# Performance work log

Measured on AMD Instinct MI355X. Metric: run time of the kernel, lower is better.

## Reference

```python
import jax, jax.numpy as jnp
import numpy as np

N_NODES = 50000
N_EDGES = 600000
IN_DIM = 128
HID = 128
OUT_DIM = 40
NUM_REL = 3
LN_EPS = 1e-5


def layer_norm(x, g, b):
    mu = jnp.mean(x, axis=-1, keepdims=True)
    var = jnp.var(x, axis=-1, keepdims=True)
    return (x - mu) * jax.lax.rsqrt(var + LN_EPS) * g + b


def rgcn_conv(x, edge_index, edge_type, w_rel, w_root, bias, aggr):
    """PyG-style RGCNConv: out = x @ W_root + bias + sum_r aggr_r(x_src @ W_r)."""
    src, dst = edge_index[0], edge_index[1]
    out = x @ w_root + bias                      # [N, F_out]
    for r in range(NUM_REL):                     # small fixed relation loop
        h = x @ w_rel[r]                         # transform-then-gather: [N, F_out]
        msg = h[src]                             # [E, F_out]
        mask = (edge_type == r)[:, None]
        if aggr == 'add':
            msg = jnp.where(mask, msg, 0.0)
            agg = jax.ops.segment_sum(msg, dst, num_segments=N_NODES)
        else:  # 'max'; empty segments -> 0 (matches PyG scatter_reduce include_self=False over zeros)
            msg = jnp.where(mask, msg, -jnp.inf)
            agg = jax.ops.segment_max(msg, dst, num_segments=N_NODES)
            agg = jnp.where(jnp.isfinite(agg), agg, 0.0)
        out = out + agg
    return out


def setup_inputs() -> dict:
    key = jax.random.key(0)
    ks = jax.random.split(key, 16)
    f32 = jnp.float32
    def lin(k, fan_in, shape):
        return jax.random.normal(k, shape, dtype=f32) / np.sqrt(fan_in)
    inp = {
        'x': jax.random.normal(ks[0], (N_NODES, IN_DIM), dtype=f32),
        'edge_index': jax.random.randint(ks[1], (2, N_EDGES), 0, N_NODES),
        'edge_type': jax.random.randint(ks[2], (N_EDGES,), 0, NUM_REL),
        # conv1
        'w1_rel': lin(ks[3], IN_DIM, (NUM_REL, IN_DIM, HID)),
        'w1_root': lin(ks[4], IN_DIM, (IN_DIM, HID)),
        'b1': jnp.zeros((HID,), f32),
        'ln1_g': jnp.ones((HID,), f32), 'ln1_b': jnp.zeros((HID,), f32),
        # conv2
        'w2_rel': lin(ks[5], HID, (NUM_REL, HID, HID)),
        'w2_root': lin(ks[6], HID, (HID, HID)),
        'b2': jnp.zeros((HID,), f32),
        'ln2_g': jnp.ones((HID,), f32), 'ln2_b': jnp.zeros((HID,), f32),
        # classifier
        'cw1': lin(ks[7], HID, (HID, HID)), 'cb1': jnp.zeros((HID,), f32),
        'cln1_g': jnp.ones((HID,), f32), 'cln1_b': jnp.zeros((HID,), f32),
        'cw2': lin(ks[8], HID, (HID, HID // 2)), 'cb2': jnp.zeros((HID // 2,), f32),
        'cln2_g': jnp.ones((HID // 2,), f32), 'cln2_b': jnp.zeros((HID // 2,), f32),
        'cw3': lin(ks[9], HID // 2, (HID // 2, OUT_DIM)), 'cb3': jnp.zeros((OUT_DIM,), f32),
    }
    return inp


def reference(x, edge_index, edge_type,
              w1_rel, w1_root, b1, ln1_g, ln1_b,
              w2_rel, w2_root, b2, ln2_g, ln2_b,
              cw1, cb1, cln1_g, cln1_b,
              cw2, cb2, cln2_g, cln2_b,
              cw3, cb3):
    # eval mode: edge dropout and feature dropout are identity
    h = rgcn_conv(x, edge_index, edge_type, w1_rel, w1_root, b1, 'add')
    h = jax.nn.relu(layer_norm(h, ln1_g, ln1_b))
    x1 = h
    h = rgcn_conv(x1, edge_index, edge_type, w2_rel, w2_root, b2, 'max')
    h = jax.nn.relu(layer_norm(h, ln2_g, ln2_b))
    h = h + x1 * 0.2
    # classifier MLP
    h = jax.nn.gelu(layer_norm(h @ cw1 + cb1, cln1_g, cln1_b), approximate=False)
    h = jax.nn.gelu(layer_norm(h @ cw2 + cb2, cln2_g, cln2_b), approximate=False)
    h = h @ cw3 + cb3
    return jax.nn.log_softmax(h, axis=1)
```

## Files before the change

kernel.cpp:

```cpp
#include <hip/hip_runtime.h>
#include <hip/hip_bf16.h>
#include <math.h>


typedef __attribute__((ext_vector_type(8))) short bf16x8;
typedef __attribute__((ext_vector_type(4))) float f32x4;
typedef unsigned short ushort_t;

__device__ __forceinline__ ushort_t bf16rne(float v) {
    unsigned u = __float_as_uint(v);
    return (ushort_t)((u + 0x7FFFu + ((u >> 16) & 1u)) >> 16);
}

__device__ __forceinline__ void split_bf16(float v, ushort_t& h, ushort_t& l) {
    ushort_t hu = bf16rne(v);
    float hf = __uint_as_float((unsigned)hu << 16);
    h = hu;
    l = bf16rne(v - hf);
}

__device__ __forceinline__ float bf2f(unsigned u16) {
    return __uint_as_float(u16 << 16);
}

__device__ __forceinline__ float4 unpack_bf4(uint2 u) {
    return make_float4(bf2f(u.x & 0xFFFFu), bf2f(u.x >> 16),
                       bf2f(u.y & 0xFFFFu), bf2f(u.y >> 16));
}

__device__ __forceinline__ uint2 pack_bf4(float4 v) {
    uint2 o;
    o.x = (unsigned)bf16rne(v.x) | ((unsigned)bf16rne(v.y) << 16);
    o.y = (unsigned)bf16rne(v.z) | ((unsigned)bf16rne(v.w) << 16);
    return o;
}

__device__ __forceinline__ void conv_body128(const float* __restrict__ W,
                                             ushort_t* __restrict__ out,
                                             int idx) {
    constexpr int NCF = 8;
    constexpr size_t PST = (size_t)4 * NCF * 512;
    int l = idx & 63;
    int cf = (idx >> 6) & 7;
    int ks = idx >> 9;
    int col = cf * 16 + (l & 15);
    int k0 = ks * 32 + (l >> 4) * 8;
    size_t base = (((size_t)ks * NCF + cf) * 64 + l) * 8;
#pragma unroll
    for (int j = 0; j < 8; ++j) {
        ushort_t h, lo_;
        split_bf16(W[(size_t)(k0 + j) * 128 + col], h, lo_);
        out[base + j] = h;
        out[PST + base + j] = lo_;
    }
}

__global__ __launch_bounds__(256) void convert_all(
    const float* __restrict__ w1_root, const float* __restrict__ w1_rel,
    const float* __restrict__ w2_root, const float* __restrict__ w2_rel,
    const float* __restrict__ cw1, const float* __restrict__ cw2,
    ushort_t* __restrict__ wfb) {
    int b = blockIdx.x;
    if (b < 72) {
        const float* src;
        int slot;
        if (b < 8)       { slot = 0;              src = w1_root; }
        else if (b < 32) { int r = (b - 8) >> 3;  slot = 1 + r; src = w1_rel + (size_t)r * 16384; }
        else if (b < 40) { slot = 4;              src = w2_root; }
        else if (b < 64) { int r = (b - 40) >> 3; slot = 5 + r; src = w2_rel + (size_t)r * 16384; }
        else             { slot = 8;              src = cw1; }
        int lb = (b < 8) ? b : (b < 32) ? ((b - 8) & 7) : (b < 40) ? (b - 32)
               : (b < 64) ? ((b - 40) & 7) : (b - 64);
        conv_body128(src, wfb + (size_t)slot * 32768, lb * 256 + threadIdx.x);
    } else {
        constexpr int NCF = 4;
        constexpr size_t PST = (size_t)4 * NCF * 512;
        int idx = (b - 72) * 256 + threadIdx.x;
        ushort_t* out = wfb + (size_t)9 * 32768;
        int l = idx & 63;
        int cf = (idx >> 6) & 3;
        int ks = idx >> 8;
        int col = cf * 16 + (l & 15);
        int k0 = ks * 32 + (l >> 4) * 8;
        size_t base = (((size_t)ks * NCF + cf) * 64 + l) * 8;
#pragma unroll
        for (int j = 0; j < 8; ++j) {
            ushort_t h, lo_;
            split_bf16(cw2[(size_t)(k0 + j) * 64 + col], h, lo_);
            out[base + j] = h;
            out[PST + base + j] = lo_;
        }
    }
}

__global__ __launch_bounds__(256) void x2bf(const float* __restrict__ x,
                                            ushort_t* __restrict__ xh, int n4) {
    int g = blockIdx.x * 256 + threadIdx.x;
    if (g >= n4) return;
    float4 v = ((const float4*)x)[g];
    ((uint2*)xh)[g] = pack_bf4(v);
}

template <int NCOL, int NSEG, int FUSE>
__global__ __launch_bounds__(256, 3) void gemm_bf(
    const ushort_t* __restrict__ A0, const ushort_t* __restrict__ A1,
    const ushort_t* __restrict__ A2, const ushort_t* __restrict__ A3,
    const ushort_t* __restrict__ wfrag, const float* __restrict__ bias,
    const float* __restrict__ lng, const float* __restrict__ lnb,
    void* __restrict__ Yv, int M) {
    constexpr int NCF = NCOL / 16;
    constexpr int WF = NCOL / 32;
    constexpr int PST = 4 * NCF * 512;
    constexpr int WSEG = 2 * PST;
    constexpr int RS = NCOL * 4 + 16;
    constexpr int EPB = 64 * RS;
    constexpr int SMEM_BYTES = (EPB > 16384) ? EPB : 16384;
    __shared__ __align__(16) char smem[SMEM_BYTES];
    char (*lds)[8192] = (char(*)[8192])smem;

    const int tid = threadIdx.x;
    const int wv = tid >> 6, lane = tid & 63, l15 = lane & 15, lg = lane >> 4;
    const int rowgrp = wv >> 1, colgrp = wv & 1;
    const int row0 = blockIdx.x * 64;
    const ushort_t* As[4] = {A0, A1, A2, A3};

    f32x4 acc[2][WF];
#pragma unroll
    for (int xf = 0; xf < 2; ++xf)
#pragma unroll
        for (int wf = 0; wf < WF; ++wf) acc[xf][wf] = (f32x4){0.f, 0.f, 0.f, 0.f};

    uint4 regs[2];

    auto LOADSTAGE = [&](int ch) {
        const ushort_t* __restrict__ A = As[ch >> 1];
        int kcb = (ch & 1) * 128;
#pragma unroll
        for (int i = 0; i < 2; ++i) {
            int s = tid + i * 256;
            int r = s >> 3, c16 = s & 7;
            int gr = row0 + r;
            uint4 v = make_uint4(0u, 0u, 0u, 0u);
            if (gr < M)
                v = *(const uint4*)((const char*)A + (size_t)gr * 256 + kcb + c16 * 16);
            regs[i] = v;
        }
    };

    auto WRITESTAGE = [&](int buf) {
        char* L = lds[buf];
#pragma unroll
        for (int i = 0; i < 2; ++i) {
            int s = tid + i * 256;
            int r = s >> 3, c16 = s & 7;
            int byte = (r * 128 + c16 * 16) ^ ((r & 7) << 4);
            *(uint4*)(L + byte) = regs[i];
        }
    };

    auto COMPUTE = [&](int ch, int buf) {
        int seg = ch >> 1, half = ch & 1;
        const ushort_t* __restrict__ ws = wfrag + (size_t)seg * WSEG;
        const char* L = lds[buf];
#pragma unroll
        for (int kk = 0; kk < 2; ++kk) {
            int ks = half * 2 + kk;
            bf16x8 xh[2];
#pragma unroll
            for (int xf = 0; xf < 2; ++xf) {
                int r = rowgrp * 32 + xf * 16 + l15;
                int byte = (r * 128 + kk * 64 + lg * 16) ^ ((r & 7) << 4);
                xh[xf] = *(const bf16x8*)(L + byte);
            }
            bf16x8 wh[WF], wl[WF];
#pragma unroll
            for (int wf = 0; wf < WF; ++wf) {
                size_t off = (((size_t)ks * NCF + colgrp * WF + wf) * 64 + lane) * 8;
                wh[wf] = *(const bf16x8*)(ws + off);
                wl[wf] = *(const bf16x8*)(ws + PST + off);
            }
#pragma unroll
            for (int xf = 0; xf < 2; ++xf)
#pragma unroll
                for (int wf = 0; wf < WF; ++wf) {
                    acc[xf][wf] = __builtin_amdgcn_mfma_f32_16x16x32_bf16(
                        wh[wf], xh[xf], acc[xf][wf], 0, 0, 0);
                    acc[xf][wf] = __builtin_amdgcn_mfma_f32_16x16x32_bf16(
                        wl[wf], xh[xf], acc[xf][wf], 0, 0, 0);
                }
        }
    };

    constexpr int CH = 2 * NSEG;
    LOADSTAGE(0);
    WRITESTAGE(0);
    __syncthreads();
    for (int ch = 0; ch < CH; ++ch) {
        if (ch + 1 < CH) LOADSTAGE(ch + 1);
        COMPUTE(ch, ch & 1);
        __syncthreads();
        if (ch + 1 < CH) WRITESTAGE((ch + 1) & 1);
        __syncthreads();
    }

    {
        float4 bv[WF];
#pragma unroll
        for (int wf = 0; wf < WF; ++wf) {
            int col = colgrp * (NCOL / 2) + wf * 16 + lg * 4;
            bv[wf] = bias ? *(const float4*)(bias + col)
                          : make_float4(0.f, 0.f, 0.f, 0.f);
        }
#pragma unroll
        for (int xf = 0; xf < 2; ++xf) {
            int r = rowgrp * 32 + xf * 16 + l15;
#pragma unroll
            for (int wf = 0; wf < WF; ++wf) {
                int col = colgrp * (NCOL / 2) + wf * 16 + lg * 4;
                float4 o;
                o.x = acc[xf][wf][0] + bv[wf].x;
                o.y = acc[xf][wf][1] + bv[wf].y;
                o.z = acc[xf][wf][2] + bv[wf].z;
                o.w = acc[xf][wf][3] + bv[wf].w;
                *(float4*)(smem + r * RS + col * 4) = o;
            }
        }
    }
    __syncthreads();

    if (FUSE >= 1 && FUSE <= 3) {
        constexpr int CPT = NCOL / 4;
        int r = tid >> 2, seg = tid & 3;
        char* rp = smem + r * RS + seg * CPT * 4;
        float s = 0.f, sq = 0.f;
        float4 vv[CPT / 4];
#pragma unroll
        for (int j = 0; j < CPT / 4; ++j) {
            float4 v = *(const float4*)(rp + j * 16);
            vv[j] = v;
            s += (v.x + v.y) + (v.z + v.w);
            sq += (v.x * v.x + v.y * v.y) + (v.z * v.z + v.w * v.w);
        }
        s += __shfl_xor(s, 1, 64); sq += __shfl_xor(sq, 1, 64);
        s += __shfl_xor(s, 2, 64); sq += __shfl_xor(sq, 2, 64);
        float mu = s * (1.f / NCOL);
        float var = sq * (1.f / NCOL) - mu * mu;
        float rstd = rsqrtf(var + 1e-5f);
#pragma unroll
        for (int j = 0; j < CPT / 4; ++j) {
            int c0 = seg * CPT + j * 4;
            float4 v = vv[j];
            float4 gg = *(const float4*)(lng + c0);
            float4 bb = *(const float4*)(lnb + c0);
            float y0 = (v.x - mu) * rstd * gg.x + bb.x;
            float y1 = (v.y - mu) * rstd * gg.y + bb.y;
            float y2 = (v.z - mu) * rstd * gg.z + bb.z;
            float y3 = (v.w - mu) * rstd * gg.w + bb.w;
            if (FUSE == 1) {
                y0 = fmaxf(y0, 0.f); y1 = fmaxf(y1, 0.f);
                y2 = fmaxf(y2, 0.f); y3 = fmaxf(y3, 0.f);
            } else {
                y0 = 0.5f * y0 * (1.f + erff(y0 * 0.70710678118654752f));
                y1 = 0.5f * y1 * (1.f + erff(y1 * 0.70710678118654752f));
                y2 = 0.5f * y2 * (1.f + erff(y2 * 0.70710678118654752f));
                y3 = 0.5f * y3 * (1.f + erff(y3 * 0.70710678118654752f));
            }
            vv[j] = make_float4(y0, y1, y2, y3);
        }
        __syncthreads();
        if (FUSE == 3) {
#pragma unroll
            for (int j = 0; j < CPT / 4; ++j) *(float4*)(rp + j * 16) = vv[j];
        } else {
#pragma unroll
            for (int j = 0; j < CPT / 4; ++j) {
                int c0 = seg * CPT + j * 4;
                *(uint2*)(smem + r * RS + 2 * c0) = pack_bf4(vv[j]);
            }
        }
        __syncthreads();
    }

    if (FUSE == 4) {
        constexpr int SL = 64 * (NCOL / 8);
#pragma unroll
        for (int i = 0; i < SL / 256; ++i) {
            int slot = tid + i * 256;
            int rr = slot / (NCOL / 8), c16 = slot % (NCOL / 8);
            int gr = row0 + rr;
            if (gr < M) {
                float4 a = *(const float4*)(smem + rr * RS + c16 * 32);
                float4 b = *(const float4*)(smem + rr * RS + c16 * 32 + 16);
                uint4 o;
                uint2 pa = pack_bf4(a), pb = pack_bf4(b);
                o.x = pa.x; o.y = pa.y; o.z = pb.x; o.w = pb.y;
                *(uint4*)((char*)Yv + (size_t)gr * (NCOL * 2) + c16 * 16) = o;
            }
        }
    } else {
        constexpr int OUTB = (FUSE == 0 || FUSE == 3) ? NCOL * 4 : NCOL * 2;
        constexpr int RP = OUTB / 16;
        constexpr int SL = 64 * RP;
#pragma unroll
        for (int i = 0; i < SL / 256; ++i) {
            int slot = tid + i * 256;
            int rr = slot / RP, c16 = slot % RP;
            int gr = row0 + rr;
            if (gr < M)
                *(uint4*)((char*)Yv + (size_t)gr * OUTB + c16 * 16) =
                    *(const uint4*)(smem + rr * RS + c16 * 16);
        }
    }
}

__global__ __launch_bounds__(256, 3) void gemm_conv2(
    const ushort_t* __restrict__ X, const ushort_t* __restrict__ wfb,
    const float* __restrict__ b2, float* __restrict__ accOut,
    ushort_t* __restrict__ H0, ushort_t* __restrict__ H1,
    ushort_t* __restrict__ H2, int M) {
    constexpr int NCF = 8, WF = 4;
    constexpr int PST = 4 * NCF * 512;
    constexpr int RS = 128 * 4 + 16;
    __shared__ __align__(16) char smem[16384 + 64 * RS];
    char* Xs = smem;
    char* ep = smem + 16384;

    const int tid = threadIdx.x;
    const int wv = tid >> 6, lane = tid & 63, l15 = lane & 15, lg = lane >> 4;
    const int rowgrp = wv >> 1, colgrp = wv & 1;
    const int row0 = blockIdx.x * 64;

#pragma unroll
    for (int i = 0; i < 4; ++i) {
        int s = tid + i * 256;
        int r = s >> 4, c16 = s & 15;
        int gr = row0 + r;
        uint4 v = make_uint4(0u, 0u, 0u, 0u);
        if (gr < M) v = *(const uint4*)((const char*)X + (size_t)gr * 256 + c16 * 16);
        int byte = (r * 256 + c16 * 16) ^ ((r & 7) << 4);
        *(uint4*)(Xs + byte) = v;
    }
    __syncthreads();

    ushort_t* Hs[3] = {H0, H1, H2};
    for (int set = 0; set < 4; ++set) {
        const ushort_t* __restrict__ ws = wfb + (size_t)(4 + set) * 32768;
        f32x4 acc[2][WF];
#pragma unroll
        for (int xf = 0; xf < 2; ++xf)
#pragma unroll
            for (int wf = 0; wf < WF; ++wf) acc[xf][wf] = (f32x4){0.f, 0.f, 0.f, 0.f};
#pragma unroll
        for (int ks = 0; ks < 4; ++ks) {
            bf16x8 xh[2];
#pragma unroll
            for (int xf = 0; xf < 2; ++xf) {
                int r = rowgrp * 32 + xf * 16 + l15;
                int byte = (r * 256 + ks * 64 + lg * 16) ^ ((r & 7) << 4);
                xh[xf] = *(const bf16x8*)(Xs + byte);
            }
            bf16x8 wh[WF], wl[WF];
#pragma unroll
            for (int wf = 0; wf < WF; ++wf) {
                size_t off = (((size_t)ks * NCF + colgrp * WF + wf) * 64 + lane) * 8;
                wh[wf] = *(const bf16x8*)(ws + off);
                wl[wf] = *(const bf16x8*)(ws + PST + off);
            }
#pragma unroll
            for (int xf = 0; xf < 2; ++xf)
#pragma unroll
                for (int wf = 0; wf < WF; ++wf) {
                    acc[xf][wf] = __builtin_amdgcn_mfma_f32_16x16x32_bf16(
                        wh[wf], xh[xf], acc[xf][wf], 0, 0, 0);
                    acc[xf][wf] = __builtin_amdgcn_mfma_f32_16x16x32_bf16(
                        wl[wf], xh[xf], acc[xf][wf], 0, 0, 0);
                }
        }
        __syncthreads();
        {
            float4 bv[WF];
#pragma unroll
            for (int wf = 0; wf < WF; ++wf) {
                int col = colgrp * 64 + wf * 16 + lg * 4;
                bv[wf] = (set == 0) ? *(const float4*)(b2 + col)
                                    : make_float4(0.f, 0.f, 0.f, 0.f);
            }
#pragma unroll
            for (int xf = 0; xf < 2; ++xf) {
                int r = rowgrp * 32 + xf * 16 + l15;
#pragma unroll
                for (int wf = 0; wf < WF; ++wf) {
                    int col = colgrp * 64 + wf * 16 + lg * 4;
                    float4 o;
                    o.x = acc[xf][wf][0] + bv[wf].x;
                    o.y = acc[xf][wf][1] + bv[wf].y;
                    o.z = acc[xf][wf][2] + bv[wf].z;
                    o.w = acc[xf][wf][3] + bv[wf].w;
                    *(float4*)(ep + r * RS + col * 4) = o;
                }
            }
        }
        __syncthreads();
        if (set == 0) {
#pragma unroll
            for (int i = 0; i < 8; ++i) {
                int slot = tid + i * 256;
                int rr = slot >> 5, c16 = slot & 31;
                int gr = row0 + rr;
                if (gr < M)
                    *(uint4*)((char*)accOut + (size_t)gr * 512 + c16 * 16) =
                        *(const uint4*)(ep + rr * RS + c16 * 16);
            }
        } else {
            ushort_t* H = Hs[set - 1];
#pragma unroll
            for (int i = 0; i < 4; ++i) {
                int slot = tid + i * 256;
                int rr = slot >> 4, c16 = slot & 15;
                int gr = row0 + rr;
                if (gr < M) {
                    float4 a = *(const float4*)(ep + rr * RS + c16 * 32);
                    float4 b = *(const float4*)(ep + rr * RS + c16 * 32 + 16);
                    uint2 pa = pack_bf4(a), pb = pack_bf4(b);
                    uint4 o; o.x = pa.x; o.y = pa.y; o.z = pb.x; o.w = pb.y;
                    *(uint4*)((char*)H + (size_t)gr * 256 + c16 * 16) = o;
                }
            }
        }
    }
}

__global__ __launch_bounds__(256) void hist3_kernel(const int* __restrict__ edst,
                                                    const int* __restrict__ etype,
                                                    int* __restrict__ deg3, int E) {
    int e = blockIdx.x * 256 + threadIdx.x;
    if (e < E) atomicAdd(&deg3[edst[e] * 3 + etype[e]], 1);
}

__global__ __launch_bounds__(256) void degtot_kernel(const int* __restrict__ deg3,
                                                     int* __restrict__ degtot, int N) {
    int n = blockIdx.x * 256 + threadIdx.x;
    if (n < N) degtot[n] = deg3[n * 3] + deg3[n * 3 + 1] + deg3[n * 3 + 2];
}

__global__ __launch_bounds__(256) void scan_block(const int* __restrict__ in,
                                                  int* __restrict__ out,
                                                  int* __restrict__ sums, int n) {
    __shared__ int s[256];
    int g = blockIdx.x * 256 + threadIdx.x;
    int v = (g < n) ? in[g] : 0;
    s[threadIdx.x] = v;
    __syncthreads();
    int acc = v;
    for (int off = 1; off < 256; off <<= 1) {
        int t = (threadIdx.x >= off) ? s[threadIdx.x - off] : 0;
        __syncthreads();
        acc += t;
        s[threadIdx.x] = acc;
        __syncthreads();
    }
    if (g < n) out[g] = acc - v;
    if (threadIdx.x == 255 && sums) sums[blockIdx.x] = acc;
}

__global__ __launch_bounds__(256) void scan_add(int* __restrict__ out,
                                                const int* __restrict__ topex,
                                                int n, int total) {
    int g = blockIdx.x * 256 + threadIdx.x;
    if (g < n) out[g] += topex[blockIdx.x];
    if (g == 0) out[n] = total;
}

__global__ __launch_bounds__(256) void ranges_kernel(
    const int* __restrict__ rowptr, const int* __restrict__ deg3,
    int4* __restrict__ ranges, int* __restrict__ cursor3, int N) {
    int n = blockIdx.x * 256 + threadIdx.x;
    if (n >= N) return;
    int b = rowptr[n];
    int d0 = deg3[n * 3], d1 = deg3[n * 3 + 1];
    int4 r;
    r.x = b; r.y = b + d0; r.z = b + d0 + d1; r.w = rowptr[n + 1];
    ranges[n] = r;
    cursor3[n * 3] = r.x; cursor3[n * 3 + 1] = r.y; cursor3[n * 3 + 2] = r.z;
}

__global__ __launch_bounds__(256) void fill3_kernel(
    const int* __restrict__ esrc, const int* __restrict__ edst,
    const int* __restrict__ etype, int* __restrict__ cursor3,
    int* __restrict__ colidx, int E) {
    int e = blockIdx.x * 256 + threadIdx.x;
    if (e >= E) return;
    int pos = atomicAdd(&cursor3[edst[e] * 3 + etype[e]], 1);
    colidx[pos] = esrc[e];
}

__device__ __forceinline__ float4 gather_sum_bf(const ushort_t* __restrict__ XH,
                                                const int* __restrict__ colidx,
                                                int beg, int end, int l) {
    float4 a = make_float4(0.f, 0.f, 0.f, 0.f);
    int e = beg;
    for (; e + 4 <= end; e += 4) {
        int s0 = colidx[e], s1 = colidx[e + 1];
        int s2 = colidx[e + 2], s3 = colidx[e + 3];
        float4 v0 = unpack_bf4(*(const uint2*)(XH + (size_t)s0 * 128 + l * 4));
        float4 v1 = unpack_bf4(*(const uint2*)(XH + (size_t)s1 * 128 + l * 4));
        float4 v2 = unpack_bf4(*(const uint2*)(XH + (size_t)s2 * 128 + l * 4));
        float4 v3 = unpack_bf4(*(const uint2*)(XH + (size_t)s3 * 128 + l * 4));
        a.x += (v0.x + v1.x) + (v2.x + v3.x);
        a.y += (v0.y + v1.y) + (v2.y + v3.y);
        a.z += (v0.z + v1.z) + (v2.z + v3.z);
        a.w += (v0.w + v1.w) + (v2.w + v3.w);
    }
    for (; e < end; ++e) {
        float4 v = unpack_bf4(*(const uint2*)(XH + (size_t)colidx[e] * 128 + l * 4));
        a.x += v.x; a.y += v.y; a.z += v.z; a.w += v.w;
    }
    return a;
}

__global__ __launch_bounds__(256) void agg3_add(
    const ushort_t* __restrict__ xh, const int4* __restrict__ ranges,
    const int* __restrict__ colidx, ushort_t* __restrict__ S0,
    ushort_t* __restrict__ S1, ushort_t* __restrict__ S2, int N) {
    int node = blockIdx.x * 8 + (threadIdx.x >> 5);
    int l = threadIdx.x & 31;
    if (node >= N) return;
    int4 rg = ranges[node];
    float4 a0 = gather_sum_bf(xh, colidx, rg.x, rg.y, l);
    float4 a1 = gather_sum_bf(xh, colidx, rg.y, rg.z, l);
    float4 a2 = gather_sum_bf(xh, colidx, rg.z, rg.w, l);
    *(uint2*)(S0 + (size_t)node * 128 + l * 4) = pack_bf4(a0);
    *(uint2*)(S1 + (size_t)node * 128 + l * 4) = pack_bf4(a1);
    *(uint2*)(S2 + (size_t)node * 128 + l * 4) = pack_bf4(a2);
}

__device__ __forceinline__ float4 gather_max_bf(const ushort_t* __restrict__ H,
                                                const int* __restrict__ colidx,
                                                int beg, int end, int l) {
    float4 m = make_float4(-INFINITY, -INFINITY, -INFINITY, -INFINITY);
    int e = beg;
    for (; e + 4 <= end; e += 4) {
        int s0 = colidx[e], s1 = colidx[e + 1];
        int s2 = colidx[e + 2], s3 = colidx[e + 3];
        float4 v0 = unpack_bf4(*(const uint2*)(H + (size_t)s0 * 128 + l * 4));
        float4 v1 = unpack_bf4(*(const uint2*)(H + (size_t)s1 * 128 + l * 4));
        float4 v2 = unpack_bf4(*(const uint2*)(H + (size_t)s2 * 128 + l * 4));
        float4 v3 = unpack_bf4(*(const uint2*)(H + (size_t)s3 * 128 + l * 4));
        m.x = fmaxf(m.x, fmaxf(fmaxf(v0.x, v1.x), fmaxf(v2.x, v3.x)));
        m.y = fmaxf(m.y, fmaxf(fmaxf(v0.y, v1.y), fmaxf(v2.y, v3.y)));
        m.z = fmaxf(m.z, fmaxf(fmaxf(v0.z, v1.z), fmaxf(v2.z, v3.z)));
        m.w = fmaxf(m.w, fmaxf(fmaxf(v0.w, v1.w), fmaxf(v2.w, v3.w)));
    }
    for (; e < end; ++e) {
        float4 v = unpack_bf4(*(const uint2*)(H + (size_t)colidx[e] * 128 + l * 4));
        m.x = fmaxf(m.x, v.x); m.y = fmaxf(m.y, v.y);
        m.z = fmaxf(m.z, v.z); m.w = fmaxf(m.w, v.w);
    }
    m.x = (m.x > -3e38f) ? m.x : 0.f;
    m.y = (m.y > -3e38f) ? m.y : 0.f;
    m.z = (m.z > -3e38f) ? m.z : 0.f;
    m.w = (m.w > -3e38f) ? m.w : 0.f;
    return m;
}

__global__ __launch_bounds__(256) void maxagg_ln(
    const ushort_t* __restrict__ H0, const ushort_t* __restrict__ H1,
    const ushort_t* __restrict__ H2, const int4* __restrict__ ranges,
    const int* __restrict__ colidx, const float* __restrict__ acc,
    const ushort_t* __restrict__ resid, const float* __restrict__ g,
    const float* __restrict__ b, ushort_t* __restrict__ outH, int N) {
    int node = blockIdx.x * 8 + (threadIdx.x >> 5);
    int l = threadIdx.x & 31;
    if (node >= N) return;
    int4 rg = ranges[node];
    float4 m0 = gather_max_bf(H0, colidx, rg.x, rg.y, l);
    float4 m1 = gather_max_bf(H1, colidx, rg.y, rg.z, l);
    float4 m2 = gather_max_bf(H2, colidx, rg.z, rg.w, l);
    float4 a = *(const float4*)(acc + (size_t)node * 128 + l * 4);
    a.x += m0.x + m1.x + m2.x;
    a.y += m0.y + m1.y + m2.y;
    a.z += m0.z + m1.z + m2.z;
    a.w += m0.w + m1.w + m2.w;
    float s = (a.x + a.y) + (a.z + a.w);
    float sq = (a.x * a.x + a.y * a.y) + (a.z * a.z + a.w * a.w);
#pragma unroll
    for (int off = 16; off; off >>= 1) {
        s += __shfl_xor(s, off, 64);
        sq += __shfl_xor(sq, off, 64);
    }
    float mu = s * (1.f / 128.f);
    float var = sq * (1.f / 128.f) - mu * mu;
    float rstd = rsqrtf(var + 1e-5f);
    float4 gg = *(const float4*)(g + l * 4);
    float4 bb = *(const float4*)(b + l * 4);
    float4 rv = unpack_bf4(*(const uint2*)(resid + (size_t)node * 128 + l * 4));
    float4 y;
    y.x = fmaxf((a.x - mu) * rstd * gg.x + bb.x, 0.f) + 0.2f * rv.x;
    y.y = fmaxf((a.y - mu) * rstd * gg.y + bb.y, 0.f) + 0.2f * rv.y;
    y.z = fmaxf((a.z - mu) * rstd * gg.z + bb.z, 0.f) + 0.2f * rv.z;
    y.w = fmaxf((a.w - mu) * rstd * gg.w + bb.w, 0.f) + 0.2f * rv.w;
    *(uint2*)(outH + (size_t)node * 128 + l * 4) = pack_bf4(y);
}

__global__ __launch_bounds__(256) void gemm40_lsm(const float* __restrict__ X,
                                                  const float* __restrict__ W,
                                                  const float* __restrict__ bias,
                                                  float* __restrict__ Y, int M) {
    __shared__ float Xs[64][65];
    __shared__ float Ws[64 * 40];
    __shared__ float Ys[64][41];
    __shared__ float mx_[64], ls_[64];
    const int tid = threadIdx.x;
    const int row0 = blockIdx.x * 64;
    for (int i = tid; i < 64 * 40; i += 256) Ws[i] = W[i];
#pragma unroll
    for (int i = 0; i < 4; ++i) {
        int slot = tid + i * 256;
        int r = slot >> 4, c4 = slot & 15;
        float4 v = make_float4(0.f, 0.f, 0.f, 0.f);
        if (row0 + r < M) v = *(const float4*)(X + (size_t)(row0 + r) * 64 + c4 * 4);
        Xs[r][c4 * 4 + 0] = v.x; Xs[r][c4 * 4 + 1] = v.y;
        Xs[r][c4 * 4 + 2] = v.z; Xs[r][c4 * 4 + 3] = v.w;
    }
    __syncthreads();
    const int row = tid >> 2, cg = (tid & 3) * 10;
    float acc[10];
#pragma unroll
    for (int j = 0; j < 10; ++j) acc[j] = 0.f;
#pragma unroll 8
    for (int k = 0; k < 64; ++k) {
        float xv = Xs[row][k];
#pragma unroll
        for (int j = 0; j < 10; ++j) acc[j] = fmaf(xv, Ws[k * 40 + cg + j], acc[j]);
    }
#pragma unroll
    for (int j = 0; j < 10; ++j) Ys[row][cg + j] = acc[j] + bias[cg + j];
    __syncthreads();
    if (tid < 64) {
        float mx = -INFINITY;
#pragma unroll 8
        for (int c = 0; c < 40; ++c) mx = fmaxf(mx, Ys[tid][c]);
        float sum = 0.f;
#pragma unroll 8
        for (int c = 0; c < 40; ++c) sum += __expf(Ys[tid][c] - mx);
        mx_[tid] = mx;
        ls_[tid] = logf(sum);
    }
    __syncthreads();
#pragma unroll
    for (int i = 0; i < 10; ++i) {
        int slot = tid + i * 256;
        int r = slot / 40, c = slot % 40;
        int gr = row0 + r;
        if (gr < M) Y[(size_t)gr * 40 + c] = Ys[r][c] - mx_[r] - ls_[r];
    }
}

extern "C" void kernel_launch(void* const* d_in, const int* in_sizes, int n_in,
                              void* d_out, int out_size, void* d_ws, size_t ws_size,
                              hipStream_t stream) {
    const float* x       = (const float*)d_in[0];
    const int*   eidx    = (const int*)d_in[1];
    const int*   etype   = (const int*)d_in[2];
    const float* w1_rel  = (const float*)d_in[3];
    const float* w1_root = (const float*)d_in[4];
    const float* b1      = (const float*)d_in[5];
    const float* ln1_g   = (const float*)d_in[6];
    const float* ln1_b   = (const float*)d_in[7];
    const float* w2_rel  = (const float*)d_in[8];
    const float* w2_root = (const float*)d_in[9];
    const float* b2      = (const float*)d_in[10];
    const float* ln2_g   = (const float*)d_in[11];
    const float* ln2_b   = (const float*)d_in[12];
    const float* cw1     = (const float*)d_in[13];
    const float* cb1     = (const float*)d_in[14];
    const float* cln1_g  = (const float*)d_in[15];
    const float* cln1_b  = (const float*)d_in[16];
    const float* cw2     = (const float*)d_in[17];
    const float* cb2     = (const float*)d_in[18];
    const float* cln2_g  = (const float*)d_in[19];
    const float* cln2_b  = (const float*)d_in[20];
    const float* cw3     = (const float*)d_in[21];
    const float* cb3     = (const float*)d_in[22];

    const int N = in_sizes[0] / 128;
    const int E = in_sizes[1] / 2;
    const int* esrc = eidx;
    const int* edst = eidx + E;

    const size_t HB = (size_t)N * 256;
    char* base = (char*)d_ws;
    ushort_t* S0 = (ushort_t*)(base + 0 * HB);
    ushort_t* S1 = (ushort_t*)(base + 1 * HB);
    ushort_t* S2 = (ushort_t*)(base + 2 * HB);
    ushort_t* X1 = (ushort_t*)(base + 3 * HB);
    float*    AC = (float*)   (base + 4 * HB);
    char*     B3 = base + 6 * HB;

    int* rowptr  = (int*)B3;
    int* degtot  = rowptr + (N + 1);
    int* deg3    = degtot + N;
    int* cursor3 = deg3 + 3 * N;
    int* bsums   = cursor3 + 3 * N;
    int* btop    = bsums + 256;
    int4* ranges = (int4*)(((uintptr_t)(btop + 256) + 15) & ~(uintptr_t)15);
    int* colidx  = (int*)(ranges + N);
    ushort_t* wfb = (ushort_t*)(((uintptr_t)(colidx + E) + 255) & ~(uintptr_t)255);
    auto WSLOT = [&](int i) { return wfb + (size_t)i * 32768; };
    ushort_t* xh = (ushort_t*)(((uintptr_t)(wfb + 10 * 32768) + 255) & ~(uintptr_t)255);
    ushort_t* h2 = xh;
    ushort_t* C1 = S0;
    float*    C2 = (float*)S1;

    const dim3 blk(256);
    const int gGemm = (N + 63) / 64;
    const int gAgg  = (N + 7) / 8;
    const int gEdge = (E + 255) / 256;
    const int gNode = (N + 255) / 256;
    const int nScanB = (N + 255) / 256;
    const int gX2  = (N * 32 + 255) / 256;

    hipMemsetAsync(deg3, 0, (size_t)3 * N * sizeof(int), stream);
    hist3_kernel<<<gEdge, blk, 0, stream>>>(edst, etype, deg3, E);
    degtot_kernel<<<gNode, blk, 0, stream>>>(deg3, degtot, N);
    scan_block<<<nScanB, blk, 0, stream>>>(degtot, rowptr, bsums, N);
    scan_block<<<1, blk, 0, stream>>>(bsums, btop, nullptr, nScanB);
    scan_add<<<nScanB, blk, 0, stream>>>(rowptr, btop, N, E);
    ranges_kernel<<<gNode, blk, 0, stream>>>(rowptr, deg3, ranges, cursor3, N);
    fill3_kernel<<<gEdge, blk, 0, stream>>>(esrc, edst, etype, cursor3, colidx, E);

    convert_all<<<76, blk, 0, stream>>>(w1_root, w1_rel, w2_root, w2_rel,
                                        cw1, cw2, wfb);
    x2bf<<<gX2, blk, 0, stream>>>(x, xh, N * 32);

    agg3_add<<<gAgg, blk, 0, stream>>>(xh, ranges, colidx, S0, S1, S2, N);
    gemm_bf<128, 4, 1><<<gGemm, blk, 0, stream>>>(
        xh, S0, S1, S2, WSLOT(0), b1, ln1_g, ln1_b, X1, N);

    gemm_conv2<<<gGemm, blk, 0, stream>>>(X1, wfb, b2, AC, S0, S1, S2, N);
    maxagg_ln<<<gAgg, blk, 0, stream>>>(S0, S1, S2, ranges, colidx, AC,
                                        X1, ln2_g, ln2_b, h2, N);

    gemm_bf<128, 1, 2><<<gGemm, blk, 0, stream>>>(
        h2, h2, h2, h2, WSLOT(8), cb1, cln1_g, cln1_b, C1, N);
    gemm_bf<64, 1, 3><<<gGemm, blk, 0, stream>>>(
        C1, C1, C1, C1, WSLOT(9), cb2, cln2_g, cln2_b, C2, N);
    gemm40_lsm<<<gGemm, blk, 0, stream>>>(C2, cw3, cb3, (float*)d_out, N);
}
```

Before: 274.5 us.

## Store conv2 root accumulator as bf16 and batch all four weight sets per k-step

```diff
diff --git a/kernel.cpp b/kernel.cpp
--- a/kernel.cpp
+++ b/kernel.cpp
@@ -313,17 +313,16 @@
     }
 }
 
-__global__ __launch_bounds__(256, 3) void gemm_conv2(
+__global__ __launch_bounds__(256, 2) void gemm_conv2(
     const ushort_t* __restrict__ X, const ushort_t* __restrict__ wfb,
-    const float* __restrict__ b2, float* __restrict__ accOut,
+    const float* __restrict__ b2, ushort_t* __restrict__ ACbf,
     ushort_t* __restrict__ H0, ushort_t* __restrict__ H1,
     ushort_t* __restrict__ H2, int M) {
     constexpr int NCF = 8, WF = 4;
     constexpr int PST = 4 * NCF * 512;
-    constexpr int RS = 128 * 4 + 16;
-    __shared__ __align__(16) char smem[16384 + 64 * RS];
+    constexpr int RS2 = 256 + 16;
+    __shared__ __align__(16) char smem[2 * 64 * RS2];
     char* Xs = smem;
-    char* ep = smem + 16384;
 
     const int tid = threadIdx.x;
     const int wv = tid >> 6, lane = tid & 63, l15 = lane & 15, lg = lane >> 4;
@@ -342,23 +341,27 @@
     }
     __syncthreads();
 
-    ushort_t* Hs[3] = {H0, H1, H2};
-    for (int set = 0; set < 4; ++set) {
-        const ushort_t* __restrict__ ws = wfb + (size_t)(4 + set) * 32768;
-        f32x4 acc[2][WF];
+    f32x4 acc[4][2][WF];
+#pragma unroll
+    for (int set = 0; set < 4; ++set)
 #pragma unroll
         for (int xf = 0; xf < 2; ++xf)
 #pragma unroll
-            for (int wf = 0; wf < WF; ++wf) acc[xf][wf] = (f32x4){0.f, 0.f, 0.f, 0.f};
-#pragma unroll
-        for (int ks = 0; ks < 4; ++ks) {
-            bf16x8 xh[2];
-#pragma unroll
-            for (int xf = 0; xf < 2; ++xf) {
-                int r = rowgrp * 32 + xf * 16 + l15;
-                int byte = (r * 256 + ks * 64 + lg * 16) ^ ((r & 7) << 4);
-                xh[xf] = *(const bf16x8*)(Xs + byte);
-            }
+            for (int wf = 0; wf < WF; ++wf)
+                acc[set][xf][wf] = (f32x4){0.f, 0.f, 0.f, 0.f};
+
+#pragma unroll
+    for (int ks = 0; ks < 4; ++ks) {
+        bf16x8 xh[2];
+#pragma unroll
+        for (int xf = 0; xf < 2; ++xf) {
+            int r = rowgrp * 32 + xf * 16 + l15;
+            int byte = (r * 256 + ks * 64 + lg * 16) ^ ((r & 7) << 4);
+            xh[xf] = *(const bf16x8*)(Xs + byte);
+        }
+#pragma unroll
+        for (int set = 0; set < 4; ++set) {
+            const ushort_t* __restrict__ ws = wfb + (size_t)(4 + set) * 32768;
             bf16x8 wh[WF], wl[WF];
 #pragma unroll
             for (int wf = 0; wf < WF; ++wf) {
@@ -370,21 +373,22 @@
             for (int xf = 0; xf < 2; ++xf)
 #pragma unroll
                 for (int wf = 0; wf < WF; ++wf) {
-                    acc[xf][wf] = __builtin_amdgcn_mfma_f32_16x16x32_bf16(
-                        wh[wf], xh[xf], acc[xf][wf], 0, 0, 0);
-                    acc[xf][wf] = __builtin_amdgcn_mfma_f32_16x16x32_bf16(
-                        wl[wf], xh[xf], acc[xf][wf], 0, 0, 0);
+                    acc[set][xf][wf] = __builtin_amdgcn_mfma_f32_16x16x32_bf16(
+                        wh[wf], xh[xf], acc[set][xf][wf], 0, 0, 0);
+                    acc[set][xf][wf] = __builtin_amdgcn_mfma_f32_16x16x32_bf16(
+                        wl[wf], xh[xf], acc[set][xf][wf], 0, 0, 0);
                 }
         }
-        __syncthreads();
-        {
-            float4 bv[WF];
-#pragma unroll
-            for (int wf = 0; wf < WF; ++wf) {
-                int col = colgrp * 64 + wf * 16 + lg * 4;
-                bv[wf] = (set == 0) ? *(const float4*)(b2 + col)
-                                    : make_float4(0.f, 0.f, 0.f, 0.f);
-            }
+    }
+    __syncthreads();
+
+    ushort_t* outs[4] = {ACbf, H0, H1, H2};
+#pragma unroll
+    for (int round = 0; round < 2; ++round) {
+#pragma unroll
+        for (int s2 = 0; s2 < 2; ++s2) {
+            int set = round * 2 + s2;
+            char* tile = smem + s2 * (64 * RS2);
 #pragma unroll
             for (int xf = 0; xf < 2; ++xf) {
                 int r = rowgrp * 32 + xf * 16 + l15;
@@ -392,41 +396,35 @@
                 for (int wf = 0; wf < WF; ++wf) {
                     int col = colgrp * 64 + wf * 16 + lg * 4;
                     float4 o;
-                    o.x = acc[xf][wf][0] + bv[wf].x;
-                    o.y = acc[xf][wf][1] + bv[wf].y;
-                    o.z = acc[xf][wf][2] + bv[wf].z;
-                    o.w = acc[xf][wf][3] + bv[wf].w;
-                    *(float4*)(ep + r * RS + col * 4) = o;
+                    o.x = acc[set][xf][wf][0];
+                    o.y = acc[set][xf][wf][1];
+                    o.z = acc[set][xf][wf][2];
+                    o.w = acc[set][xf][wf][3];
+                    if (set == 0) {
+                        float4 bv = *(const float4*)(b2 + col);
+                        o.x += bv.x; o.y += bv.y; o.z += bv.z; o.w += bv.w;
+                    }
+                    *(uint2*)(tile + r * RS2 + col * 2) = pack_bf4(o);
                 }
             }
         }
         __syncthreads();
-        if (set == 0) {
-#pragma unroll
-            for (int i = 0; i < 8; ++i) {
-                int slot = tid + i * 256;
-                int rr = slot >> 5, c16 = slot & 31;
-                int gr = row0 + rr;
-                if (gr < M)
-                    *(uint4*)((char*)accOut + (size_t)gr * 512 + c16 * 16) =
-                        *(const uint4*)(ep + rr * RS + c16 * 16);
-            }
-        } else {
-            ushort_t* H = Hs[set - 1];
+#pragma unroll
+        for (int s2 = 0; s2 < 2; ++s2) {
+            int set = round * 2 + s2;
+            ushort_t* O = outs[set];
+            const char* tile = smem + s2 * (64 * RS2);
 #pragma unroll
             for (int i = 0; i < 4; ++i) {
                 int slot = tid + i * 256;
                 int rr = slot >> 4, c16 = slot & 15;
                 int gr = row0 + rr;
-                if (gr < M) {
-                    float4 a = *(const float4*)(ep + rr * RS + c16 * 32);
-                    float4 b = *(const float4*)(ep + rr * RS + c16 * 32 + 16);
-                    uint2 pa = pack_bf4(a), pb = pack_bf4(b);
-                    uint4 o; o.x = pa.x; o.y = pa.y; o.z = pb.x; o.w = pb.y;
-                    *(uint4*)((char*)H + (size_t)gr * 256 + c16 * 16) = o;
-                }
-            }
-        }
+                if (gr < M)
+                    *(uint4*)((char*)O + (size_t)gr * 256 + c16 * 16) =
+                        *(const uint4*)(tile + rr * RS2 + c16 * 16);
+            }
+        }
+        if (round == 0) __syncthreads();
     }
 }
 
@@ -566,7 +564,7 @@
 __global__ __launch_bounds__(256) void maxagg_ln(
     const ushort_t* __restrict__ H0, const ushort_t* __restrict__ H1,
     const ushort_t* __restrict__ H2, const int4* __restrict__ ranges,
-    const int* __restrict__ colidx, const float* __restrict__ acc,
+    const int* __restrict__ colidx, const ushort_t* __restrict__ accbf,
     const ushort_t* __restrict__ resid, const float* __restrict__ g,
     const float* __restrict__ b, ushort_t* __restrict__ outH, int N) {
     int node = blockIdx.x * 8 + (threadIdx.x >> 5);
@@ -576,7 +574,7 @@
     float4 m0 = gather_max_bf(H0, colidx, rg.x, rg.y, l);
     float4 m1 = gather_max_bf(H1, colidx, rg.y, rg.z, l);
     float4 m2 = gather_max_bf(H2, colidx, rg.z, rg.w, l);
-    float4 a = *(const float4*)(acc + (size_t)node * 128 + l * 4);
+    float4 a = unpack_bf4(*(const uint2*)(accbf + (size_t)node * 128 + l * 4));
     a.x += m0.x + m1.x + m2.x;
     a.y += m0.y + m1.y + m2.y;
     a.z += m0.z + m1.z + m2.z;
@@ -694,8 +692,8 @@
     ushort_t* S1 = (ushort_t*)(base + 1 * HB);
     ushort_t* S2 = (ushort_t*)(base + 2 * HB);
     ushort_t* X1 = (ushort_t*)(base + 3 * HB);
-    float*    AC = (float*)   (base + 4 * HB);
-    char*     B3 = base + 6 * HB;
+    ushort_t* AC = (ushort_t*)(base + 4 * HB);
+    char*     B3 = base + 5 * HB;
 
     int* rowptr  = (int*)B3;
     int* degtot  = rowptr + (N + 1);
```

New measurement: 289.8 us. 5.6% more time.
